# Kernel tuning notes

Hardware: AMD Instinct MI355X
Metric: run time of the kernel (lower is better)

The kernel has to match this reference:

```python
import jax, jax.numpy as jnp
import numpy as np

N_SEG = 8192
AVG_LEN = 128
D = 64
TOTAL = N_SEG * AVG_LEN  # 1,048,576 rows


def _make_lengths():
    # Variable segment lengths in [68, 188] that sum exactly to TOTAL.
    rng = np.random.default_rng(0)
    delta = rng.integers(-60, 61, size=N_SEG // 2)
    lengths = np.concatenate([AVG_LEN + delta, AVG_LEN - delta]).astype(np.int64)
    rng.shuffle(lengths)
    assert lengths.sum() == TOTAL
    return lengths


def setup_inputs() -> dict:
    key = jax.random.key(0)
    data = jax.random.normal(key, (TOTAL, D), dtype=jnp.float32)
    lengths = jnp.asarray(_make_lengths())
    return {"data": data, "lengths": lengths}


def reference(data, lengths):
    # aten.segment_reduce(data, 'sum', lengths=lengths, axis=0, initial=0.0):
    # out[s] = initial + sum of data rows belonging to segment s (ragged, contiguous).
    n_seg = lengths.shape[0]
    seg_ids = jnp.repeat(jnp.arange(n_seg), lengths, total_repeat_length=data.shape[0])
    out = jax.ops.segment_sum(data, seg_ids, num_segments=n_seg)  # [n_seg, D]
    return out  # initial = 0.0 adds nothing
```

## Files before the change

kernel.cpp:

```cpp
#include <hip/hip_runtime.h>
#include <hip/hip_bf16.h>


__global__ __launch_bounds__(256) void seg_sum_fused(
    const float* __restrict__ data, const int* __restrict__ lengths,
    float* __restrict__ out, int n_seg) {
    const int tid = threadIdx.x;
    const int wave = tid >> 6;
    const int lane = tid & 63;
    const int s0 = blockIdx.x * 4;

    const int n4 = s0 >> 2;
    const int4* __restrict__ l4 = reinterpret_cast<const int4*>(lengths);
    int psum = 0;
    for (int i = tid; i < n4; i += 256) {
        int4 v = l4[i];
        psum += v.x + v.y + v.z + v.w;
    }
    #pragma unroll
    for (int off = 32; off >= 1; off >>= 1) psum += __shfl_down(psum, off);

    __shared__ int wsum[4];
    if (lane == 0) wsum[wave] = psum;
    __syncthreads();
    const int S = wsum[0] + wsum[1] + wsum[2] + wsum[3];

    const int s = s0 + wave;
    if (s >= n_seg) return;

    int start = S;
    for (int j = 0; j < wave; ++j) start += lengths[s0 + j];
    const int len = lengths[s];

    const int c = lane & 15;
    const int rg = lane >> 4;

    const float4* __restrict__ base =
        reinterpret_cast<const float4*>(data) + (size_t)start * 16 + c;

    float4 a0 = make_float4(0.f, 0.f, 0.f, 0.f);
    float4 a1 = make_float4(0.f, 0.f, 0.f, 0.f);

    int r = rg;
    for (; r + 4 < len; r += 8) {
        float4 v0 = base[(size_t)r * 16];
        float4 v1 = base[(size_t)(r + 4) * 16];
        a0.x += v0.x; a0.y += v0.y; a0.z += v0.z; a0.w += v0.w;
        a1.x += v1.x; a1.y += v1.y; a1.z += v1.z; a1.w += v1.w;
    }
    if (r < len) {
        float4 v0 = base[(size_t)r * 16];
        a0.x += v0.x; a0.y += v0.y; a0.z += v0.z; a0.w += v0.w;
    }
    a0.x += a1.x; a0.y += a1.y; a0.z += a1.z; a0.w += a1.w;

    #pragma unroll
    for (int off = 32; off >= 16; off >>= 1) {
        a0.x += __shfl_down(a0.x, off);
        a0.y += __shfl_down(a0.y, off);
        a0.z += __shfl_down(a0.z, off);
        a0.w += __shfl_down(a0.w, off);
    }

    if (rg == 0) {
        reinterpret_cast<float4*>(out)[(size_t)s * 16 + c] = a0;
    }
}

extern "C" void kernel_launch(void* const* d_in, const int* in_sizes, int n_in,
                              void* d_out, int out_size, void* d_ws, size_t ws_size,
                              hipStream_t stream) {
    const float* data = (const float*)d_in[0];
    const int* lengths = (const int*)d_in[1];
    const int n_seg = in_sizes[1];
    float* out = (float*)d_out;

    const int grid = (n_seg + 3) / 4;
    seg_sum_fused<<<grid, 256, 0, stream>>>(data, lengths, out, n_seg);
}
```

Measured before the change: 47.95 us.

## Process eight segments per block, cache lengths in LDS, unroll row loop 4x

```diff
diff --git a/kernel.cpp b/kernel.cpp
--- a/kernel.cpp
+++ b/kernel.cpp
@@ -2,57 +2,75 @@
 #include <hip/hip_bf16.h>
 
 
-__global__ __launch_bounds__(256) void seg_sum_fused(
+__global__ __launch_bounds__(512) void seg_sum_fused(
     const float* __restrict__ data, const int* __restrict__ lengths,
     float* __restrict__ out, int n_seg) {
     const int tid = threadIdx.x;
     const int wave = tid >> 6;
     const int lane = tid & 63;
-    const int s0 = blockIdx.x * 4;
+    const int s0 = blockIdx.x * 8;
+
+    __shared__ int wsum[8];
+    __shared__ int slen[8];
+
+    if (tid < 8) {
+        int idx = s0 + tid;
+        slen[tid] = (idx < n_seg) ? lengths[idx] : 0;
+    }
 
     const int n4 = s0 >> 2;
     const int4* __restrict__ l4 = reinterpret_cast<const int4*>(lengths);
     int psum = 0;
-    for (int i = tid; i < n4; i += 256) {
+    for (int i = tid; i < n4; i += 512) {
         int4 v = l4[i];
         psum += v.x + v.y + v.z + v.w;
     }
     #pragma unroll
     for (int off = 32; off >= 1; off >>= 1) psum += __shfl_down(psum, off);
-
-    __shared__ int wsum[4];
     if (lane == 0) wsum[wave] = psum;
     __syncthreads();
-    const int S = wsum[0] + wsum[1] + wsum[2] + wsum[3];
+
+    int S = 0;
+    #pragma unroll
+    for (int j = 0; j < 8; ++j) S += wsum[j];
 
     const int s = s0 + wave;
     if (s >= n_seg) return;
 
     int start = S;
-    for (int j = 0; j < wave; ++j) start += lengths[s0 + j];
-    const int len = lengths[s];
+    for (int j = 0; j < wave; ++j) start += slen[j];
+    const int len = slen[wave];
 
     const int c = lane & 15;
     const int rg = lane >> 4;
 
-    const float4* __restrict__ base =
-        reinterpret_cast<const float4*>(data) + (size_t)start * 16 + c;
+    const float4* __restrict__ p =
+        reinterpret_cast<const float4*>(data) + (size_t)(start + rg) * 16 + c;
 
     float4 a0 = make_float4(0.f, 0.f, 0.f, 0.f);
     float4 a1 = make_float4(0.f, 0.f, 0.f, 0.f);
+    float4 a2 = make_float4(0.f, 0.f, 0.f, 0.f);
+    float4 a3 = make_float4(0.f, 0.f, 0.f, 0.f);
 
     int r = rg;
-    for (; r + 4 < len; r += 8) {
-        float4 v0 = base[(size_t)r * 16];
-        float4 v1 = base[(size_t)(r + 4) * 16];
+    for (; r + 12 < len; r += 16, p += 256) {
+        float4 v0 = p[0];
+        float4 v1 = p[64];
+        float4 v2 = p[128];
+        float4 v3 = p[192];
         a0.x += v0.x; a0.y += v0.y; a0.z += v0.z; a0.w += v0.w;
         a1.x += v1.x; a1.y += v1.y; a1.z += v1.z; a1.w += v1.w;
+        a2.x += v2.x; a2.y += v2.y; a2.z += v2.z; a2.w += v2.w;
+        a3.x += v3.x; a3.y += v3.y; a3.z += v3.z; a3.w += v3.w;
     }
-    if (r < len) {
-        float4 v0 = base[(size_t)r * 16];
+    for (; r < len; r += 4, p += 64) {
+        float4 v0 = p[0];
         a0.x += v0.x; a0.y += v0.y; a0.z += v0.z; a0.w += v0.w;
     }
-    a0.x += a1.x; a0.y += a1.y; a0.z += a1.z; a0.w += a1.w;
+    a0.x += a1.x + a2.x + a3.x;
+    a0.y += a1.y + a2.y + a3.y;
+    a0.z += a1.z + a2.z + a3.z;
+    a0.w += a1.w + a2.w + a3.w;
 
     #pragma unroll
     for (int off = 32; off >= 16; off >>= 1) {
@@ -75,6 +93,6 @@
     const int n_seg = in_sizes[1];
     float* out = (float*)d_out;
 
-    const int grid = (n_seg + 3) / 4;
-    seg_sum_fused<<<grid, 256, 0, stream>>>(data, lengths, out, n_seg);
+    const int grid = (n_seg + 7) / 8;
+    seg_sum_fused<<<grid, 512, 0, stream>>>(data, lengths, out, n_seg);
 }
```

Result: no change. 47.23 us, median of 2 (-1.5%).
